# Kernel optimization log

Hardware: AMD Instinct MI355X
Metric: run time of the kernel (lower is better)

Reference implementation:

```python
import jax, jax.numpy as jnp
import numpy as np

B, S, D = 2, 2048, 512
H = 8
HD = D // H
SCALES = (1, 2, 4)


def setup_inputs() -> dict:
    key = jax.random.key(0)
    ks = jax.random.split(key, 7)
    std = 1.0 / np.sqrt(D)
    return {
        "x": jax.random.normal(ks[0], (B, S, D), dtype=jnp.float32),
        "Wq": jax.random.normal(ks[1], (D, D), dtype=jnp.float32) * std,
        "bq": jax.random.normal(ks[2], (D,), dtype=jnp.float32) * std,
        "Wk": jax.random.normal(ks[3], (D, D), dtype=jnp.float32) * std,
        "bk": jax.random.normal(ks[4], (D,), dtype=jnp.float32) * std,
        "Wv": jax.random.normal(ks[5], (D, D), dtype=jnp.float32) * std,
        "bv": jax.random.normal(ks[6], (D,), dtype=jnp.float32) * std,
    }


def _positional_encoding(seq_len, d):
    # Matches torch: pos[:,None] / 10000**(arange(0,d,2)/d), then cat(sin, cos) -> [S, d]
    pos = jnp.arange(seq_len, dtype=jnp.float32)[:, None]
    inv = 10000.0 ** (jnp.arange(0, d, 2, dtype=jnp.float32) / d)
    ang = pos / inv  # [S, d/2]
    return jnp.concatenate([jnp.sin(ang), jnp.cos(ang)], axis=-1)  # [S, d]


def reference(x, Wq, bq, Wk, bk, Wv, bv):
    b, s, d = x.shape
    x = x + _positional_encoding(s, d)[None]
    q = x @ Wq + bq
    k = x @ Wk + bk
    v = x @ Wv + bv
    qh = q.reshape(b, s, H, HD).transpose(0, 2, 1, 3)  # [B,H,S,HD]
    scale = HD ** -0.5
    outs = []
    for sc in SCALES:
        kh = k[:, ::sc].reshape(b, -1, H, HD).transpose(0, 2, 1, 3)  # [B,H,S/sc,HD]
        vh = v[:, ::sc].reshape(b, -1, H, HD).transpose(0, 2, 1, 3)
        scores = jnp.einsum("bhqd,bhkd->bhqk", qh, kh) * scale
        w = jax.nn.softmax(scores, axis=-1)  # dropout p=0 -> identity
        outs.append(jnp.einsum("bhqk,bhkd->bhqd", w, vh))
    out = jnp.mean(jnp.stack(outs, axis=-2), axis=-2)  # mean over scales
    return out.transpose(0, 2, 1, 3).reshape(b, s, d)
```

## Files before the change

kernel.cpp:

```cpp
#include <hip/hip_runtime.h>
#include <hip/hip_fp16.h>

typedef _Float16 half8 __attribute__((ext_vector_type(8)));
typedef _Float16 half4v __attribute__((ext_vector_type(4)));
typedef __fp16 fp16x2 __attribute__((ext_vector_type(2)));
typedef __fp16 fp16x4 __attribute__((ext_vector_type(4)));
typedef float f32x4 __attribute__((ext_vector_type(4)));

static constexpr int SS = 2048, DD = 512;
static constexpr int MM = 2 * SS;
static constexpr int PAD = 72;

__device__ __forceinline__ void stage16(const _Float16* g, _Float16* l) {
    __builtin_amdgcn_global_load_lds(
        (const __attribute__((address_space(1))) unsigned int*)g,
        (__attribute__((address_space(3))) unsigned int*)l,
        16, 0, 0);
}

__device__ __forceinline__ float exp2v(float x) {
#if __has_builtin(__builtin_amdgcn_exp2f)
    return __builtin_amdgcn_exp2f(x);
#else
    float r;
    asm("v_exp_f32 %0, %1\n\ts_nop 0" : "=v"(r) : "v"(x));
    return r;
#endif
}

__global__ __launch_bounds__(256) void pe_kernel(const float* __restrict__ x,
                                                 _Float16* __restrict__ xb) {
    int idx = blockIdx.x * 256 + threadIdx.x;
    if (idx >= MM * DD) return;
    int d = idx & (DD - 1);
    int s = (idx >> 9) & (SS - 1);
    int dd = d & 255;
    float p = __expf(-(float)dd * 0.03597789207803197f);
    float ang = (float)s * p;
    float pe = (d < 256) ? sinf(ang) : cosf(ang);
    xb[idx] = (_Float16)(x[idx] + pe);
}

__global__ __launch_bounds__(256) void wt_kernel(const float* __restrict__ Wq,
                                                 const float* __restrict__ Wk,
                                                 const float* __restrict__ Wv,
                                                 _Float16* __restrict__ WbT) {
    __shared__ float tile[64][65];
    int tk = blockIdx.x;
    int tn = blockIdx.y;
    const float* W = (tn < 8) ? Wq : (tn < 16) ? Wk : Wv;
    int nbase = (tn & 7) * 64;
    int t = threadIdx.x;
    for (int i = 0; i < 16; ++i) {
        int e = t + i * 256;
        int row = e >> 6, col = e & 63;
        tile[row][col] = W[(tk * 64 + row) * 512 + nbase + col];
    }
    __syncthreads();
    for (int i = 0; i < 16; ++i) {
        int e = t + i * 256;
        int row = e >> 6, col = e & 63;
        WbT[(size_t)(tn * 64 + row) * 512 + tk * 64 + col] = (_Float16)tile[col][row];
    }
}

__global__ __launch_bounds__(256) void qkv_gemm(
    const _Float16* __restrict__ xb, const _Float16* __restrict__ WbT,
    const float* __restrict__ bq, const float* __restrict__ bk, const float* __restrict__ bv,
    _Float16* __restrict__ qbuf,
    _Float16* __restrict__ k1, _Float16* __restrict__ k2, _Float16* __restrict__ k4,
    _Float16* __restrict__ v1, _Float16* __restrict__ v2, _Float16* __restrict__ v4)
{
    __shared__ _Float16 As[128][PAD];
    __shared__ _Float16 Bs[128][PAD];
    int bm = blockIdx.x, bn = blockIdx.y;
    int t = threadIdx.x;
    int w = t >> 6, lane = t & 63;
    int wm = w >> 1, wn = w & 1;
    int l15 = lane & 15, lg = lane >> 4;

    f32x4 zero = {0.f, 0.f, 0.f, 0.f};
    f32x4 acc[4][4];
    for (int i = 0; i < 4; ++i)
        for (int j = 0; j < 4; ++j) acc[i][j] = zero;

    for (int kt = 0; kt < 8; ++kt) {
        for (int i = 0; i < 4; ++i) {
            int e = t + i * 256;
            int row = e >> 3, c8 = (e & 7) * 8;
            *(half8*)&As[row][c8] =
                *(const half8*)&xb[(size_t)(bm * 128 + row) * 512 + kt * 64 + c8];
            *(half8*)&Bs[row][c8] =
                *(const half8*)&WbT[(size_t)(bn * 128 + row) * 512 + kt * 64 + c8];
        }
        __syncthreads();
        for (int kk = 0; kk < 2; ++kk) {
            half8 af[4], bf[4];
            for (int mi = 0; mi < 4; ++mi)
                af[mi] = *(const half8*)&As[wm * 64 + mi * 16 + l15][kk * 32 + lg * 8];
            for (int ni = 0; ni < 4; ++ni)
                bf[ni] = *(const half8*)&Bs[wn * 64 + ni * 16 + l15][kk * 32 + lg * 8];
            for (int mi = 0; mi < 4; ++mi)
                for (int ni = 0; ni < 4; ++ni)
                    acc[mi][ni] = __builtin_amdgcn_mfma_f32_16x16x32_f16(
                        af[mi], bf[ni], acc[mi][ni], 0, 0, 0);
        }
        __syncthreads();
    }

    int colbase = bn * 128 + wn * 64;
    int rowbase = bm * 128 + wm * 64;
    for (int ni = 0; ni < 4; ++ni) {
        int n = colbase + ni * 16 + l15;
        float bias = (n < 512) ? bq[n] : (n < 1024) ? bk[n - 512] : bv[n - 1024];
        for (int mi = 0; mi < 4; ++mi) {
            for (int r = 0; r < 4; ++r) {
                int m = rowbase + mi * 16 + lg * 4 + r;
                float val = acc[mi][ni][r] + bias;
                _Float16 hv = (_Float16)val;
                int b = m >> 11, s = m & 2047;
                if (n < 512) {
                    qbuf[(size_t)m * 512 + n] = hv;
                } else if (n < 1024) {
                    int nk = n - 512, h = nk >> 6, hd = nk & 63, bh = b * 8 + h;
                    k1[((size_t)bh * 2048 + s) * 64 + hd] = hv;
                    if ((s & 1) == 0) k2[((size_t)bh * 1024 + (s >> 1)) * 64 + hd] = hv;
                    if ((s & 3) == 0) k4[((size_t)bh * 512 + (s >> 2)) * 64 + hd] = hv;
                } else {
                    int nv = n - 1024, h = nv >> 6, hd = nv & 63, bh = b * 8 + h;
                    v1[((size_t)bh * 64 + hd) * 2048 + s] = hv;
                    if ((s & 1) == 0) v2[((size_t)bh * 64 + hd) * 1024 + (s >> 1)] = hv;
                    if ((s & 3) == 0) v4[((size_t)bh * 64 + hd) * 512 + (s >> 2)] = hv;
                }
            }
        }
    }
}

__global__ __launch_bounds__(256, 4) void attn_kernel(
    const _Float16* __restrict__ qbuf,
    const _Float16* __restrict__ k1, const _Float16* __restrict__ k2, const _Float16* __restrict__ k4,
    const _Float16* __restrict__ v1, const _Float16* __restrict__ v2, const _Float16* __restrict__ v4,
    _Float16* __restrict__ numA, _Float16* __restrict__ numB,
    _Float16* __restrict__ n1, _Float16* __restrict__ n2,
    float* __restrict__ denA, float* __restrict__ denB)
{
    __shared__ alignas(16) _Float16 Ks[2][4096];
    __shared__ alignas(16) _Float16 Vs[2][4096];

    int bid = blockIdx.x;
    int g = bid >> 8;
    int rr = bid & 255;
    int qb = rr >> 4, bh = rr & 15;
    int b = bh >> 3, h = bh & 7;
    int t = threadIdx.x, w = t >> 6, lane = t & 63;
    int l15 = lane & 15, lg = lane >> 4;
    int qbase = qb * 128 + w * 32;
    int sw = l15 & 7;

    const _Float16 qscale = (_Float16)0.18033688f;
    half8 qf[2][2];
#pragma unroll
    for (int f = 0; f < 2; ++f)
#pragma unroll
        for (int kk = 0; kk < 2; ++kk) {
            half8 v = *(const half8*)&qbuf[((size_t)(b * 2048 + qbase + f * 16 + l15)) * 512
                                           + h * 64 + kk * 32 + lg * 8];
#pragma unroll
            for (int j = 0; j < 8; ++j) v[j] = v[j] * qscale;
            qf[f][kk] = v;
        }

    const _Float16* kptr[3] = {k1, k2, k4};
    const _Float16* vptr[3] = {v1, v2, v4};
    const int si = (g < 2) ? 0 : (g - 1);
    const int kb0 = (g == 1) ? 16 : 0;
    const int ntiles = (g == 3) ? 8 : 16;
    const int Sk = 2048 >> si;
    const _Float16* kbase = kptr[si] + ((size_t)bh * Sk + kb0 * 64) * 64;
    const _Float16* vbase = vptr[si] + (size_t)bh * 64 * Sk + kb0 * 64;

    auto stage = [&](int buf, int tt) {
        const _Float16* kpT = kbase + tt * 4096;
        const _Float16* vpT = vbase + tt * 64;
#pragma unroll
        for (int p = 0; p < 2; ++p) {
            int id = (w * 2 + p) * 64 + lane;
            int row = id >> 3, ch = id & 7;
            stage16(kpT + row * 64 + ((ch ^ (row & 7)) << 3), &Ks[buf][(w * 2 + p) * 512]);
        }
#pragma unroll
        for (int p = 0; p < 2; ++p) {
            int id = (w * 2 + p) * 64 + lane;
            int row = id >> 3, ch = id & 7;
            stage16(vpT + (size_t)row * Sk + ((ch ^ (row & 7)) << 3), &Vs[buf][(w * 2 + p) * 512]);
        }
    };

    const float einit = -5.770780163f;
    f32x4 szero = {einit, einit, einit, einit};
    f32x4 zero = {0.f, 0.f, 0.f, 0.f};
    float psum[2] = {0.f, 0.f};
    f32x4 oacc[2][4];
#pragma unroll
    for (int f = 0; f < 2; ++f)
#pragma unroll
        for (int hc = 0; hc < 4; ++hc) oacc[f][hc] = zero;

    stage(0, 0);
    __syncthreads();
    int cur = 0;
    for (int tt = 0; tt < ntiles; ++tt) {
        if (tt + 1 < ntiles) stage(cur ^ 1, tt + 1);
        const _Float16* Kc = &Ks[cur][0];
        const _Float16* Vc = &Vs[cur][0];
        __builtin_amdgcn_s_setprio(1);

        f32x4 sacc[2][4];
#pragma unroll
        for (int f = 0; f < 2; ++f)
#pragma unroll
            for (int c = 0; c < 4; ++c) sacc[f][c] = szero;
#pragma unroll
        for (int c = 0; c < 4; ++c) {
            int row = c * 16 + l15;
            half8 kf0 = *(const half8*)&Kc[row * 64 + ((lg ^ sw) << 3)];
            half8 kf1 = *(const half8*)&Kc[row * 64 + (((lg + 4) ^ sw) << 3)];
#pragma unroll
            for (int f = 0; f < 2; ++f) {
                sacc[f][c] = __builtin_amdgcn_mfma_f32_16x16x32_f16(kf0, qf[f][0], sacc[f][c], 0, 0, 0);
                sacc[f][c] = __builtin_amdgcn_mfma_f32_16x16x32_f16(kf1, qf[f][1], sacc[f][c], 0, 0, 0);
            }
        }

        half4v pa[2][4];
#pragma unroll
        for (int f = 0; f < 2; ++f)
#pragma unroll
            for (int c = 0; c < 4; ++c) {
                float p0 = exp2v(sacc[f][c][0]);
                float p1 = exp2v(sacc[f][c][1]);
                float p2 = exp2v(sacc[f][c][2]);
                float p3 = exp2v(sacc[f][c][3]);
                psum[f] += (p0 + p1) + (p2 + p3);
                fp16x2 lo = __builtin_amdgcn_cvt_pkrtz(p0, p1);
                fp16x2 hi = __builtin_amdgcn_cvt_pkrtz(p2, p3);
                fp16x4 pk4 = __builtin_shufflevector(lo, hi, 0, 1, 2, 3);
                pa[f][c] = __builtin_bit_cast(half4v, pk4);
            }

#pragma unroll
        for (int hc = 0; hc < 4; ++hc) {
            int vrow = hc * 16 + l15;
#pragma unroll
            for (int c = 0; c < 4; ++c) {
                int chb = 2 * c + (lg >> 1);
                half4v vb = *(const half4v*)&Vc[vrow * 64 + ((chb ^ sw) << 3) + ((lg & 1) << 2)];
                oacc[0][hc] = __builtin_amdgcn_mfma_f32_16x16x16f16(pa[0][c], vb, oacc[0][hc], 0, 0, 0);
                oacc[1][hc] = __builtin_amdgcn_mfma_f32_16x16x16f16(pa[1][c], vb, oacc[1][hc], 0, 0, 0);
            }
        }
        __builtin_amdgcn_s_setprio(0);
        __syncthreads();
        cur ^= 1;
    }

    if (g < 2) {
        _Float16* po = g ? numB : numA;
        float* dp = g ? denB : denA;
#pragma unroll
        for (int f = 0; f < 2; ++f) {
            float tot = psum[f];
            tot += __shfl_xor(tot, 16);
            tot += __shfl_xor(tot, 32);
            if (lg == 0)
                dp[((size_t)(b * 2048 + qbase + f * 16 + l15)) * 8 + h] = tot;
#pragma unroll
            for (int hc = 0; hc < 4; ++hc)
#pragma unroll
                for (int r = 0; r < 4; ++r) {
                    int s = qbase + f * 16 + lg * 4 + r;
                    po[((size_t)(b * 2048 + s)) * 512 + h * 64 + hc * 16 + l15] =
                        (_Float16)oacc[f][hc][r];
                }
        }
    } else {
        _Float16* po = (g == 2) ? n1 : n2;
#pragma unroll
        for (int f = 0; f < 2; ++f) {
            float tot = psum[f];
            tot += __shfl_xor(tot, 16);
            tot += __shfl_xor(tot, 32);
            float linv = 1.0f / tot;
            float lr[4];
#pragma unroll
            for (int r = 0; r < 4; ++r) lr[r] = __shfl(linv, lg * 4 + r, 16);
#pragma unroll
            for (int hc = 0; hc < 4; ++hc)
#pragma unroll
                for (int r = 0; r < 4; ++r) {
                    int s = qbase + f * 16 + lg * 4 + r;
                    po[((size_t)(b * 2048 + s)) * 512 + h * 64 + hc * 16 + l15] =
                        (_Float16)(oacc[f][hc][r] * lr[r]);
                }
        }
    }
}

__global__ __launch_bounds__(256) void combine_kernel(
    const _Float16* __restrict__ numA, const _Float16* __restrict__ numB,
    const _Float16* __restrict__ n1, const _Float16* __restrict__ n2,
    const float* __restrict__ denA, const float* __restrict__ denB,
    float* __restrict__ out) {
    int idx = blockIdx.x * 256 + threadIdx.x;
    const size_t N = (size_t)MM * DD;
    size_t off = (size_t)idx * 8;
    if (off >= N) return;
    int bs = (int)(off >> 9);
    int h = (int)(off >> 6) & 7;
    float dinv = 1.0f / (denA[bs * 8 + h] + denB[bs * 8 + h]);
    half8 a = *(const half8*)&numA[off];
    half8 bb = *(const half8*)&numB[off];
    half8 c = *(const half8*)&n1[off];
    half8 d = *(const half8*)&n2[off];
    const float third = 1.0f / 3.0f;
    float o[8];
#pragma unroll
    for (int j = 0; j < 8; ++j)
        o[j] = (((float)a[j] + (float)bb[j]) * dinv + (float)c[j] + (float)d[j]) * third;
    *(f32x4*)&out[off] = *(f32x4*)&o[0];
    *(f32x4*)&out[off + 4] = *(f32x4*)&o[4];
}

extern "C" void kernel_launch(void* const* d_in, const int* in_sizes, int n_in,
                              void* d_out, int out_size, void* d_ws, size_t ws_size,
                              hipStream_t stream) {
    const float* x  = (const float*)d_in[0];
    const float* Wq = (const float*)d_in[1];
    const float* bq = (const float*)d_in[2];
    const float* Wk = (const float*)d_in[3];
    const float* bk = (const float*)d_in[4];
    const float* Wv = (const float*)d_in[5];
    const float* bv = (const float*)d_in[6];
    float* out = (float*)d_out;

    char* ws = (char*)d_ws;
    _Float16* xb   = (_Float16*)ws; ws += (size_t)4096 * 512 * 2;
    _Float16* WbT  = (_Float16*)ws; ws += (size_t)1536 * 512 * 2;
    _Float16* qbuf = (_Float16*)ws; ws += (size_t)4096 * 512 * 2;
    _Float16* k1   = (_Float16*)ws; ws += (size_t)16 * 2048 * 64 * 2;
    _Float16* k2   = (_Float16*)ws; ws += (size_t)16 * 1024 * 64 * 2;
    _Float16* k4   = (_Float16*)ws; ws += (size_t)16 * 512 * 64 * 2;
    _Float16* v1   = (_Float16*)ws; ws += (size_t)16 * 2048 * 64 * 2;
    _Float16* v2   = (_Float16*)ws; ws += (size_t)16 * 1024 * 64 * 2;
    _Float16* v4   = (_Float16*)ws; ws += (size_t)16 * 512 * 64 * 2;
    _Float16* numA = (_Float16*)ws; ws += (size_t)4096 * 512 * 2;
    _Float16* numB = (_Float16*)ws; ws += (size_t)4096 * 512 * 2;
    _Float16* n1   = (_Float16*)ws; ws += (size_t)4096 * 512 * 2;
    _Float16* n2   = (_Float16*)ws; ws += (size_t)4096 * 512 * 2;
    float*    denA = (float*)ws;    ws += (size_t)4096 * 8 * 4;
    float*    denB = (float*)ws;    ws += (size_t)4096 * 8 * 4;

    hipLaunchKernelGGL(pe_kernel, dim3(8192), dim3(256), 0, stream, x, xb);
    hipLaunchKernelGGL(wt_kernel, dim3(8, 24), dim3(256), 0, stream, Wq, Wk, Wv, WbT);
    hipLaunchKernelGGL(qkv_gemm, dim3(32, 12), dim3(256), 0, stream,
                       xb, WbT, bq, bk, bv, qbuf, k1, k2, k4, v1, v2, v4);
    hipLaunchKernelGGL(attn_kernel, dim3(1024), dim3(256), 0, stream,
                       qbuf, k1, k2, k4, v1, v2, v4, numA, numB, n1, n2, denA, denB);
    hipLaunchKernelGGL(combine_kernel, dim3(1024), dim3(256), 0, stream,
                       numA, numB, n1, n2, denA, denB, out);
}
```

Baseline: 83.84 us.

## Double-buffer QKV GEMM with async LDS loads, smaller tiles, vectorize PE kernel

The QKV projection GEMM now stages tiles into double-buffered LDS using direct global-to-LDS loads with an XOR swizzle, so the next K-tile's loads overlap the current tile's MFMAs. Its M tile shrinks from 128 to 64, doubling the grid to fill more CUs, and the bias selection is hoisted per block. The positional-encoding kernel is vectorized to 8 elements per thread with fast sin/cos intrinsics. Fast __sinf/__cosf on large angles (up to 2047) may lose accuracy, and the smaller tiles reduce data reuse per block.

```diff
diff --git a/kernel.cpp b/kernel.cpp
--- a/kernel.cpp
+++ b/kernel.cpp
@@ -9,7 +9,6 @@
 
 static constexpr int SS = 2048, DD = 512;
 static constexpr int MM = 2 * SS;
-static constexpr int PAD = 72;
 
 __device__ __forceinline__ void stage16(const _Float16* g, _Float16* l) {
     __builtin_amdgcn_global_load_lds(
@@ -31,14 +30,26 @@
 __global__ __launch_bounds__(256) void pe_kernel(const float* __restrict__ x,
                                                  _Float16* __restrict__ xb) {
     int idx = blockIdx.x * 256 + threadIdx.x;
-    if (idx >= MM * DD) return;
-    int d = idx & (DD - 1);
-    int s = (idx >> 9) & (SS - 1);
-    int dd = d & 255;
-    float p = __expf(-(float)dd * 0.03597789207803197f);
-    float ang = (float)s * p;
-    float pe = (d < 256) ? sinf(ang) : cosf(ang);
-    xb[idx] = (_Float16)(x[idx] + pe);
+    int row = idx >> 6;
+    int s = row & (SS - 1);
+    int d0 = (idx & 63) * 8;
+    size_t off = (size_t)row * 512 + d0;
+    f32x4 x0 = *(const f32x4*)&x[off];
+    f32x4 x1 = *(const f32x4*)&x[off + 4];
+    bool issin = d0 < 256;
+    float fs = (float)s;
+    half8 o;
+#pragma unroll
+    for (int j = 0; j < 8; ++j) {
+        int d = d0 + j;
+        int dd = d & 255;
+        float p = __expf(-(float)dd * 0.03597789207803197f);
+        float ang = fs * p;
+        float pe = issin ? __sinf(ang) : __cosf(ang);
+        float xv = (j < 4) ? x0[j] : x1[j - 4];
+        o[j] = (_Float16)(xv + pe);
+    }
+    *(half8*)&xb[off] = o;
 }
 
 __global__ __launch_bounds__(256) void wt_kernel(const float* __restrict__ Wq,
@@ -64,70 +75,108 @@
     }
 }
 
-__global__ __launch_bounds__(256) void qkv_gemm(
+__global__ __launch_bounds__(256, 3) void qkv_gemm(
     const _Float16* __restrict__ xb, const _Float16* __restrict__ WbT,
     const float* __restrict__ bq, const float* __restrict__ bk, const float* __restrict__ bv,
     _Float16* __restrict__ qbuf,
     _Float16* __restrict__ k1, _Float16* __restrict__ k2, _Float16* __restrict__ k4,
     _Float16* __restrict__ v1, _Float16* __restrict__ v2, _Float16* __restrict__ v4)
 {
-    __shared__ _Float16 As[128][PAD];
-    __shared__ _Float16 Bs[128][PAD];
-    int bm = blockIdx.x, bn = blockIdx.y;
+    __shared__ alignas(16) _Float16 As[2][64 * 64];
+    __shared__ alignas(16) _Float16 Bs[2][128 * 64];
+    int bm = blockIdx.x;
+    int bn = blockIdx.y;
     int t = threadIdx.x;
     int w = t >> 6, lane = t & 63;
     int wm = w >> 1, wn = w & 1;
     int l15 = lane & 15, lg = lane >> 4;
 
+    const _Float16* asrc[2];
+#pragma unroll
+    for (int i = 0; i < 2; ++i) {
+        int id = t + i * 256;
+        int row = id >> 3, p = id & 7;
+        asrc[i] = xb + (size_t)(bm * 64 + row) * 512 + ((p ^ (row & 7)) << 3);
+    }
+    const _Float16* bsrc[4];
+#pragma unroll
+    for (int i = 0; i < 4; ++i) {
+        int id = t + i * 256;
+        int row = id >> 3, p = id & 7;
+        bsrc[i] = WbT + (size_t)(bn * 128 + row) * 512 + ((p ^ (row & 7)) << 3);
+    }
+
+    auto stage = [&](int buf, int kt) {
+#pragma unroll
+        for (int i = 0; i < 2; ++i)
+            stage16(asrc[i] + kt * 64, &As[buf][(w * 64 + i * 256) * 8]);
+#pragma unroll
+        for (int i = 0; i < 4; ++i)
+            stage16(bsrc[i] + kt * 64, &Bs[buf][(w * 64 + i * 256) * 8]);
+    };
+
     f32x4 zero = {0.f, 0.f, 0.f, 0.f};
-    f32x4 acc[4][4];
-    for (int i = 0; i < 4; ++i)
+    f32x4 acc[2][4];
+#pragma unroll
+    for (int i = 0; i < 2; ++i)
+#pragma unroll
         for (int j = 0; j < 4; ++j) acc[i][j] = zero;
 
+    stage(0, 0);
+    __syncthreads();
+    int cur = 0;
     for (int kt = 0; kt < 8; ++kt) {
-        for (int i = 0; i < 4; ++i) {
-            int e = t + i * 256;
-            int row = e >> 3, c8 = (e & 7) * 8;
-            *(half8*)&As[row][c8] =
-                *(const half8*)&xb[(size_t)(bm * 128 + row) * 512 + kt * 64 + c8];
-            *(half8*)&Bs[row][c8] =
-                *(const half8*)&WbT[(size_t)(bn * 128 + row) * 512 + kt * 64 + c8];
-        }
-        __syncthreads();
+        if (kt + 1 < 8) stage(cur ^ 1, kt + 1);
+        const _Float16* Ac = &As[cur][0];
+        const _Float16* Bc = &Bs[cur][0];
+#pragma unroll
         for (int kk = 0; kk < 2; ++kk) {
-            half8 af[4], bf[4];
-            for (int mi = 0; mi < 4; ++mi)
-                af[mi] = *(const half8*)&As[wm * 64 + mi * 16 + l15][kk * 32 + lg * 8];
-            for (int ni = 0; ni < 4; ++ni)
-                bf[ni] = *(const half8*)&Bs[wn * 64 + ni * 16 + l15][kk * 32 + lg * 8];
-            for (int mi = 0; mi < 4; ++mi)
+            int ch = kk * 4 + lg;
+            half8 af[2], bf[4];
+#pragma unroll
+            for (int mi = 0; mi < 2; ++mi) {
+                int row = wm * 32 + mi * 16 + l15;
+                af[mi] = *(const half8*)&Ac[row * 64 + ((ch ^ (row & 7)) << 3)];
+            }
+#pragma unroll
+            for (int ni = 0; ni < 4; ++ni) {
+                int row = wn * 64 + ni * 16 + l15;
+                bf[ni] = *(const half8*)&Bc[row * 64 + ((ch ^ (row & 7)) << 3)];
+            }
+#pragma unroll
+            for (int mi = 0; mi < 2; ++mi)
+#pragma unroll
                 for (int ni = 0; ni < 4; ++ni)
                     acc[mi][ni] = __builtin_amdgcn_mfma_f32_16x16x32_f16(
                         af[mi], bf[ni], acc[mi][ni], 0, 0, 0);
         }
         __syncthreads();
-    }
-
-    int colbase = bn * 128 + wn * 64;
-    int rowbase = bm * 128 + wm * 64;
+        cur ^= 1;
+    }
+
+    int which = bn >> 2;
+    const float* bias_p = (which == 0) ? bq : (which == 1) ? bk : bv;
+#pragma unroll
     for (int ni = 0; ni < 4; ++ni) {
-        int n = colbase + ni * 16 + l15;
-        float bias = (n < 512) ? bq[n] : (n < 1024) ? bk[n - 512] : bv[n - 1024];
-        for (int mi = 0; mi < 4; ++mi) {
+        int n = (bn & 3) * 128 + wn * 64 + ni * 16 + l15;
+        float bias = bias_p[n];
+#pragma unroll
+        for (int mi = 0; mi < 2; ++mi) {
+#pragma unroll
             for (int r = 0; r < 4; ++r) {
-                int m = rowbase + mi * 16 + lg * 4 + r;
+                int m = bm * 64 + wm * 32 + mi * 16 + lg * 4 + r;
                 float val = acc[mi][ni][r] + bias;
                 _Float16 hv = (_Float16)val;
                 int b = m >> 11, s = m & 2047;
-                if (n < 512) {
+                if (which == 0) {
                     qbuf[(size_t)m * 512 + n] = hv;
-                } else if (n < 1024) {
-                    int nk = n - 512, h = nk >> 6, hd = nk & 63, bh = b * 8 + h;
+                } else if (which == 1) {
+                    int h = n >> 6, hd = n & 63, bh = b * 8 + h;
                     k1[((size_t)bh * 2048 + s) * 64 + hd] = hv;
                     if ((s & 1) == 0) k2[((size_t)bh * 1024 + (s >> 1)) * 64 + hd] = hv;
                     if ((s & 3) == 0) k4[((size_t)bh * 512 + (s >> 2)) * 64 + hd] = hv;
                 } else {
-                    int nv = n - 1024, h = nv >> 6, hd = nv & 63, bh = b * 8 + h;
+                    int h = n >> 6, hd = n & 63, bh = b * 8 + h;
                     v1[((size_t)bh * 64 + hd) * 2048 + s] = hv;
                     if ((s & 1) == 0) v2[((size_t)bh * 64 + hd) * 1024 + (s >> 1)] = hv;
                     if ((s & 3) == 0) v4[((size_t)bh * 64 + hd) * 512 + (s >> 2)] = hv;
@@ -361,9 +410,9 @@
     float*    denA = (float*)ws;    ws += (size_t)4096 * 8 * 4;
     float*    denB = (float*)ws;    ws += (size_t)4096 * 8 * 4;
 
-    hipLaunchKernelGGL(pe_kernel, dim3(8192), dim3(256), 0, stream, x, xb);
+    hipLaunchKernelGGL(pe_kernel, dim3(1024), dim3(256), 0, stream, x, xb);
     hipLaunchKernelGGL(wt_kernel, dim3(8, 24), dim3(256), 0, stream, Wq, Wk, Wv, WbT);
-    hipLaunchKernelGGL(qkv_gemm, dim3(32, 12), dim3(256), 0, stream,
+    hipLaunchKernelGGL(qkv_gemm, dim3(64, 12), dim3(256), 0, stream,
                        xb, WbT, bq, bk, bv, qbuf, k1, k2, k4, v1, v2, v4);
     hipLaunchKernelGGL(attn_kernel, dim3(1024), dim3(256), 0, stream,
                        qbuf, k1, k2, k4, v1, v2, v4, numA, numB, n1, n2, denA, denB);
```

Result: faster. 75.36 us (-10.1%).
